# Kernel tuning notes

Hardware: AMD Instinct MI355X
Metric: run time of the kernel (lower is better)

## Reference

```python
import jax, jax.numpy as jnp
import numpy as np

# Production-scale dims (see shape_source)
B, L, K = 4096, 5, 32            # batch, hyperedge length (col0=cell id), neighbors/row
N = B * (L - 1)                  # aggregation rows = 16384
U, V = 131072, 500000            # unique neighbor nodes, embedding vocab (total bins)
F, E = 256, 256                  # feat_dim, embed_dim


def setup_inputs() -> dict:
    key = jax.random.key(0)
    ks = jax.random.split(key, 6)
    nodes = jax.random.randint(ks[0], (B, L), 0, V)                      # [B,L] int
    mask_row = jnp.repeat(jnp.arange(N, dtype=jnp.int32), K)             # [N*K] COO rows
    mask_col = jax.random.randint(ks[1], (N * K,), 0, U)                 # [N*K] COO cols
    mask_val = jnp.full((N * K,), 1.0 / K, dtype=jnp.float32)            # mean weights 1/deg
    unique_nodes = jax.random.randint(ks[2], (U,), 0, V)                 # [U] node ids
    embed_table = jax.random.normal(ks[3], (V, F), dtype=jnp.float32) * 0.02
    W = jax.random.normal(ks[4], (E, 2 * F), dtype=jnp.float32) / np.sqrt(2 * F)
    b = jnp.zeros((E,), dtype=jnp.float32)
    return dict(nodes=nodes, mask_row=mask_row, mask_col=mask_col, mask_val=mask_val,
                unique_nodes=unique_nodes, embed_table=embed_table, W=W, b=b)


def reference(nodes, mask_row, mask_col, mask_val, unique_nodes, embed_table, W, b):
    sz_b, len_seq = nodes.shape
    nodes_flat = nodes[:, 1:].reshape(-1)                                # [N]
    # MeanAggregator_with_weights: embed_matrix = features(unique_nodes)
    embed_matrix = embed_table[unique_nodes]                             # [U,F]
    # mask.mm(embed_matrix): COO spmm == gather + weighted segment-sum
    gathered = embed_matrix[mask_col] * mask_val[:, None]                # [nnz,F]
    neigh_feats = jax.ops.segment_sum(gathered, mask_row, num_segments=N)  # [N,F]
    # gcn=False -> concat self features (GraphSAGE-style)
    self_feats = embed_table[nodes_flat]                                 # [N,F]
    combined = jnp.concatenate([neigh_feats, self_feats], axis=-1)       # [N,2F]
    # swish(Linear(combined))
    h = combined @ W.T + b
    h = h * jax.nn.sigmoid(h)                                            # swish
    h = h.reshape(sz_b, len_seq - 1, -1)                                 # [B,L-1,E]
    # cell features from column 0, prepended
    cell_feats = embed_table[nodes[:, 0]]                                # [B,F]
    return jnp.concatenate([cell_feats[:, None, :], h], axis=1)          # [B,L,E]
```

## Files before the change

kernel.cpp:

```cpp
#include <hip/hip_runtime.h>
#include <math.h>

typedef float f4     __attribute__((ext_vector_type(4)));
typedef float f32x4  __attribute__((ext_vector_type(4)));
typedef short bf16x8 __attribute__((ext_vector_type(8)));
typedef unsigned short u16x4 __attribute__((ext_vector_type(4)));
typedef unsigned int   u32x4 __attribute__((ext_vector_type(4)));

#define NROWS   16384
#define KNEI    32
#define FDIM    256
#define TWOF    512
#define EDIM    256
#define BATCH   4096
#define UROWS   131072
#define BM      32

static __device__ __forceinline__ unsigned short f2bf(float x) {
    union { float f; unsigned int i; } c; c.f = x;
    unsigned int u = c.i;
    u += 0x7fffu + ((u >> 16) & 1u);
    return (unsigned short)(u >> 16);
}


#define EMBED_PB   2048
#define CELL_PB    64
#define WCONV_PB   8
#define ROWS_PW    16

__global__ __launch_bounds__(256) void prep_kernel(
    const int* __restrict__ unique_nodes, const float* __restrict__ table,
    const int* __restrict__ nodes, const float* __restrict__ W,
    unsigned short* __restrict__ embed4, float* __restrict__ scales,
    float* __restrict__ out, unsigned short* __restrict__ Wb)
{
    const int wave = threadIdx.x >> 6;
    const int lane = threadIdx.x & 63;
    const int blk  = blockIdx.x;

    if (blk < EMBED_PB) {
        const int u0 = (blk * 4 + wave) * ROWS_PW;
        #pragma unroll 2
        for (int t = 0; t < ROWS_PW; ++t) {
            const int u   = u0 + t;
            const int row = unique_nodes[u];
            const f4 e = *(const f4*)(table + (size_t)row * FDIM + lane * 4);
            float m = fmaxf(fmaxf(fabsf(e[0]), fabsf(e[1])),
                            fmaxf(fabsf(e[2]), fabsf(e[3])));
            #pragma unroll
            for (int s = 1; s < 64; s <<= 1)
                m = fmaxf(m, __shfl_xor(m, s));
            m = fmaxf(m, 1e-30f);
            const float inv = 7.0f / m;
            unsigned short pk = 0;
            #pragma unroll
            for (int j = 0; j < 4; ++j) {
                float qf = __builtin_rintf(e[j] * inv);
                qf = fminf(fmaxf(qf, -7.0f), 7.0f);
                const int q = (int)qf;
                pk |= (unsigned short)((q & 0xF) << (4 * j));
            }
            embed4[((size_t)u << 6) + lane] = pk;
            if (lane == 0) scales[u] = m * (1.0f / 7.0f);
        }
    } else if (blk < EMBED_PB + CELL_PB) {
        const int b0 = ((blk - EMBED_PB) * 4 + wave) * ROWS_PW;
        #pragma unroll 4
        for (int t = 0; t < ROWS_PW; ++t) {
            const int b = b0 + t;
            const int node = nodes[b * 5];
            const f4 e = *(const f4*)(table + (size_t)node * FDIM + lane * 4);
            *(f4*)(out + (size_t)b * 5 * FDIM + lane * 4) = e;
        }
    } else {
        const int base = (blk - EMBED_PB - CELL_PB) * 256 * 16 + threadIdx.x;
        #pragma unroll 4
        for (int t = 0; t < 16; ++t) {
            const int idx = base + t * 256;
            const f4 w = *(const f4*)(W + (size_t)idx * 4);
            u16x4 o;
            #pragma unroll
            for (int j = 0; j < 4; ++j) o[j] = f2bf(w[j]);
            *(u16x4*)(Wb + (size_t)idx * 4) = o;
        }
    }
}

__global__ __launch_bounds__(512, 4) void fused_kernel(
    const int* __restrict__ mask_col, const float* __restrict__ mask_val,
    const unsigned int* __restrict__ embed4, const float* __restrict__ scales,
    const int* __restrict__ nodes, const float* __restrict__ table,
    const unsigned short* __restrict__ Wb, const float* __restrict__ bias,
    float* __restrict__ out)
{
    __shared__ unsigned short As[BM * TWOF];
    char* const As_b = (char*)As;

    const int wave  = threadIdx.x >> 6;
    const int lane  = threadIdx.x & 63;
    const int half  = lane >> 5;
    const int l32   = lane & 31;
    const int rbase = blockIdx.x * BM;

    #pragma unroll
    for (int p = 0; p < 2; ++p) {
        const int lr = wave * 4 + p * 2;
        const int gi = rbase + lr;

        const int j   = gi * KNEI + lane;
        const int col = mask_col[j];
        const float val = mask_val[j] * scales[col];

        const int i_g = gi + half;
        const int nfr = nodes[(i_g >> 2) * 5 + 1 + (i_g & 3)];
        const float* sp = table + (size_t)nfr * FDIM + l32 * 8;
        const f4 s0 = *(const f4*)sp;
        const f4 s1 = *(const f4*)(sp + 4);

        f4 accA = (f4){0.f,0.f,0.f,0.f};
        f4 accB = (f4){0.f,0.f,0.f,0.f};
        #pragma unroll 8
        for (int k = 0; k < KNEI; ++k) {
            const int   c = __shfl(col, (lane & 32) + k);
            const float v = __shfl(val, (lane & 32) + k);
            const unsigned int w = embed4[((size_t)c << 5) + l32];
            #pragma unroll
            for (int d = 0; d < 4; ++d) {
                const int qa = ((int)(w << (28 - 4 * d))) >> 28;
                const int qb = ((int)(w << (12 - 4 * d))) >> 28;
                accA[d] += v * (float)qa;
                accB[d] += v * (float)qb;
            }
        }

        const int lrow = lr + half;
        const int swz  = (lrow & 7) << 4;

        u32x4 on;
        on[0] = (unsigned)f2bf(accA[0]) | ((unsigned)f2bf(accA[1]) << 16);
        on[1] = (unsigned)f2bf(accA[2]) | ((unsigned)f2bf(accA[3]) << 16);
        on[2] = (unsigned)f2bf(accB[0]) | ((unsigned)f2bf(accB[1]) << 16);
        on[3] = (unsigned)f2bf(accB[2]) | ((unsigned)f2bf(accB[3]) << 16);
        *(u32x4*)(As_b + lrow * 1024 + ((l32 * 16) ^ swz)) = on;

        u32x4 os;
        os[0] = (unsigned)f2bf(s0[0]) | ((unsigned)f2bf(s0[1]) << 16);
        os[1] = (unsigned)f2bf(s0[2]) | ((unsigned)f2bf(s0[3]) << 16);
        os[2] = (unsigned)f2bf(s1[0]) | ((unsigned)f2bf(s1[1]) << 16);
        os[3] = (unsigned)f2bf(s1[2]) | ((unsigned)f2bf(s1[3]) << 16);
        *(u32x4*)(As_b + lrow * 1024 + ((512 + l32 * 16) ^ swz)) = os;
    }

    __syncthreads();

    const int n_w    = wave * 32;
    const int lrow16 = lane & 15;
    const int koff   = (lane >> 4) * 8;
    const int aswz   = (lrow16 & 7) << 4;

    f32x4 acc[2][2] = {};
    const unsigned short* wp = Wb + (size_t)(n_w + lrow16) * TWOF + koff;

    #pragma unroll 4
    for (int kb = 0; kb < TWOF; kb += 32) {
        const int kbyte = (koff + kb) * 2;
        const bf16x8 a0 = *(const bf16x8*)(As_b + (lrow16     ) * 1024 + (kbyte ^ aswz));
        const bf16x8 a1 = *(const bf16x8*)(As_b + (lrow16 + 16) * 1024 + (kbyte ^ aswz));
        const bf16x8 b0 = *(const bf16x8*)(wp + kb);
        const bf16x8 b1 = *(const bf16x8*)(wp + 16 * TWOF + kb);
        acc[0][0] = __builtin_amdgcn_mfma_f32_16x16x32_bf16(a0, b0, acc[0][0], 0, 0, 0);
        acc[0][1] = __builtin_amdgcn_mfma_f32_16x16x32_bf16(a0, b1, acc[0][1], 0, 0, 0);
        acc[1][0] = __builtin_amdgcn_mfma_f32_16x16x32_bf16(a1, b0, acc[1][0], 0, 0, 0);
        acc[1][1] = __builtin_amdgcn_mfma_f32_16x16x32_bf16(a1, b1, acc[1][1], 0, 0, 0);
    }

    float bn[2];
    #pragma unroll
    for (int ni = 0; ni < 2; ++ni) bn[ni] = bias[n_w + ni * 16 + lrow16];

    #pragma unroll
    for (int mi = 0; mi < 2; ++mi) {
        #pragma unroll
        for (int ni = 0; ni < 2; ++ni) {
            const int n = n_w + ni * 16 + lrow16;
            #pragma unroll
            for (int j = 0; j < 4; ++j) {
                const int i = rbase + mi * 16 + (lane >> 4) * 4 + j;
                float h = acc[mi][ni][j] + bn[ni];
                h = h / (1.0f + __expf(-h));
                out[((size_t)(i >> 2) * 5 + 1 + (i & 3)) * FDIM + n] = h;
            }
        }
    }
}

__global__ __launch_bounds__(256) void neigh_f32_kernel(
    const int* __restrict__ mask_col, const float* __restrict__ mask_val,
    const int* __restrict__ unique_nodes, const float* __restrict__ table,
    float* __restrict__ neigh)
{
    const int wave = threadIdx.x >> 6;
    const int lane = threadIdx.x & 63;
    const int i = blockIdx.x * 4 + wave;
    int   row_l = 0;
    float val_l = 0.0f;
    if (lane < KNEI) {
        const int j = i * KNEI + lane;
        const int c = mask_col[j];
        val_l = mask_val[j];
        row_l = unique_nodes[c];
    }
    f4 acc = (f4){0.f, 0.f, 0.f, 0.f};
    #pragma unroll 8
    for (int k = 0; k < KNEI; ++k) {
        const int   row = __shfl(row_l, k);
        const float v   = __shfl(val_l, k);
        const f4 e = *(const f4*)(table + (size_t)row * FDIM + lane * 4);
        acc += v * e;
    }
    *(f4*)(neigh + (size_t)i * FDIM + lane * 4) = acc;
}

__global__ __launch_bounds__(256) void cell_kernel(
    const int* __restrict__ nodes, const float* __restrict__ table,
    float* __restrict__ out)
{
    const int wave = threadIdx.x >> 6;
    const int lane = threadIdx.x & 63;
    const int b = blockIdx.x * 4 + wave;
    const int node = nodes[b * 5];
    const f4 e = *(const f4*)(table + (size_t)node * FDIM + lane * 4);
    *(f4*)(out + (size_t)b * 5 * FDIM + lane * 4) = e;
}

__global__ __launch_bounds__(256) void gemm_f32_kernel(
    const float* __restrict__ neigh, const float* __restrict__ table,
    const int* __restrict__ nodes, const float* __restrict__ W,
    const float* __restrict__ bias, float* __restrict__ out)
{
    __shared__ float Asf[16][64];
    __shared__ float Wsf[16][64];
    const int t  = threadIdx.x;
    const int i0 = blockIdx.x * 64;
    const int e0 = blockIdx.y * 64;
    const int r  = t >> 2;
    const int k4 = (t & 3) << 2;
    const int irow = i0 + r;
    const int nfr = nodes[(irow >> 2) * 5 + 1 + (irow & 3)];
    const int tm = (t >> 4) << 2;
    const int tn = (t & 15) << 2;
    float acc[4][4] = {};
    for (int kb = 0; kb < TWOF; kb += 16) {
        const float* asrc = (kb < FDIM)
            ? (neigh + (size_t)irow * FDIM + kb + k4)
            : (table + (size_t)nfr  * FDIM + (kb - FDIM) + k4);
        const f4 av = *(const f4*)asrc;
        const f4 wv = *(const f4*)(W + (size_t)(e0 + r) * TWOF + kb + k4);
        __syncthreads();
        #pragma unroll
        for (int j = 0; j < 4; ++j) { Asf[k4 + j][r] = av[j]; Wsf[k4 + j][r] = wv[j]; }
        __syncthreads();
        #pragma unroll
        for (int k = 0; k < 16; ++k) {
            const f4 a = *(const f4*)&Asf[k][tm];
            const f4 w = *(const f4*)&Wsf[k][tn];
            #pragma unroll
            for (int mi = 0; mi < 4; ++mi)
                #pragma unroll
                for (int ni = 0; ni < 4; ++ni)
                    acc[mi][ni] += a[mi] * w[ni];
        }
    }
    #pragma unroll
    for (int mi = 0; mi < 4; ++mi) {
        const int i  = i0 + tm + mi;
        float* op = out + ((size_t)(i >> 2) * 5 + 1 + (i & 3)) * FDIM + e0 + tn;
        f4 hv;
        #pragma unroll
        for (int ni = 0; ni < 4; ++ni) {
            const float h = acc[mi][ni] + bias[e0 + tn + ni];
            hv[ni] = h / (1.0f + __expf(-h));
        }
        *(f4*)op = hv;
    }
}

extern "C" void kernel_launch(void* const* d_in, const int* in_sizes, int n_in,
                              void* d_out, int out_size, void* d_ws, size_t ws_size,
                              hipStream_t stream)
{
    const int*   nodes        = (const int*)  d_in[0];
    const int*   mask_col     = (const int*)  d_in[2];
    const float* mask_val     = (const float*)d_in[3];
    const int*   unique_nodes = (const int*)  d_in[4];
    const float* table        = (const float*)d_in[5];
    const float* W            = (const float*)d_in[6];
    const float* bias         = (const float*)d_in[7];
    float*       out          = (float*)d_out;

    const size_t EMBED4_B = (size_t)UROWS * 128;
    const size_t SC_B     = (size_t)UROWS * 4;
    const size_t W_B      = (size_t)EDIM  * TWOF * 2;

    if (ws_size >= EMBED4_B + SC_B + W_B) {
        unsigned short* embed4 = (unsigned short*)d_ws;
        float*          scales = (float*)((char*)d_ws + EMBED4_B);
        unsigned short* Wb     = (unsigned short*)((char*)d_ws + EMBED4_B + SC_B);

        prep_kernel<<<EMBED_PB + CELL_PB + WCONV_PB, 256, 0, stream>>>(
            unique_nodes, table, nodes, W, embed4, scales, out, Wb);
        fused_kernel<<<NROWS / BM, 512, 0, stream>>>(
            mask_col, mask_val, (const unsigned int*)embed4, scales,
            nodes, table, Wb, bias, out);
    } else {
        float* neigh = (float*)d_ws;
        neigh_f32_kernel<<<NROWS / 4, 256, 0, stream>>>(mask_col, mask_val,
                                                        unique_nodes, table, neigh);
        cell_kernel     <<<BATCH / 4, 256, 0, stream>>>(nodes, table, out);
        gemm_f32_kernel <<<dim3(NROWS / 64, EDIM / 64), 256, 0, stream>>>(
            neigh, table, nodes, W, bias, out);
    }
}
```

Measured before the change: 60.52 us.

## Fuse prep and main kernels with a grid barrier and offset-encoded int4 decode

Merges the embedding quantization, cell-feature copy and W-to-bf16 conversion into the main fused kernel. Each block does its share of prep work, then all blocks wait on a global atomic-counter barrier before the aggregation and GEMM phase. The int4 packing now stores nibbles with a +8 offset in an interleaved layout, so decoding is a mask-and-shift instead of sign-extending shifts; the offset is removed afterwards using the sum of the weights. The barrier assumes all 512 blocks are resident at once and adds a memset launch plus spin-wait cost.

```diff
diff --git a/kernel.cpp b/kernel.cpp
--- a/kernel.cpp
+++ b/kernel.cpp
@@ -15,6 +15,7 @@
 #define BATCH   4096
 #define UROWS   131072
 #define BM      32
+#define NBLK    (NROWS / BM)
 
 static __device__ __forceinline__ unsigned short f2bf(float x) {
     union { float f; unsigned int i; } c; c.f = x;
@@ -23,85 +24,79 @@
     return (unsigned short)(u >> 16);
 }
 
-
-#define EMBED_PB   2048
-#define CELL_PB    64
-#define WCONV_PB   8
-#define ROWS_PW    16
-
-__global__ __launch_bounds__(256) void prep_kernel(
-    const int* __restrict__ unique_nodes, const float* __restrict__ table,
-    const int* __restrict__ nodes, const float* __restrict__ W,
-    unsigned short* __restrict__ embed4, float* __restrict__ scales,
-    float* __restrict__ out, unsigned short* __restrict__ Wb)
-{
+__global__ __launch_bounds__(512, 4) void mega_kernel(
+    const int* __restrict__ mask_col, const float* __restrict__ mask_val,
+    const int* __restrict__ unique_nodes, const int* __restrict__ nodes,
+    const float* __restrict__ table, const float* __restrict__ W,
+    const float* __restrict__ bias,
+    unsigned int* __restrict__ embed4, float* __restrict__ scales,
+    unsigned short* __restrict__ Wb, unsigned int* __restrict__ ctrl,
+    float* __restrict__ out)
+{
+    __shared__ unsigned short As[BM * TWOF];
+    char* const As_b = (char*)As;
+
+    const int bid  = blockIdx.x;
     const int wave = threadIdx.x >> 6;
     const int lane = threadIdx.x & 63;
-    const int blk  = blockIdx.x;
-
-    if (blk < EMBED_PB) {
-        const int u0 = (blk * 4 + wave) * ROWS_PW;
+    const int half = lane >> 5;
+    const int l32  = lane & 31;
+
+    {
+        const int u0 = bid * 256 + wave * 32;
         #pragma unroll 2
-        for (int t = 0; t < ROWS_PW; ++t) {
-            const int u   = u0 + t;
+        for (int t = 0; t < 16; ++t) {
+            const int u   = u0 + t * 2 + half;
             const int row = unique_nodes[u];
-            const f4 e = *(const f4*)(table + (size_t)row * FDIM + lane * 4);
-            float m = fmaxf(fmaxf(fabsf(e[0]), fabsf(e[1])),
-                            fmaxf(fabsf(e[2]), fabsf(e[3])));
-            #pragma unroll
-            for (int s = 1; s < 64; s <<= 1)
-                m = fmaxf(m, __shfl_xor(m, s));
+            const float* rp = table + (size_t)row * FDIM + l32 * 8;
+            const f4 e0 = *(const f4*)rp;
+            const f4 e1 = *(const f4*)(rp + 4);
+            float m = fmaxf(
+                fmaxf(fmaxf(fabsf(e0[0]), fabsf(e0[1])), fmaxf(fabsf(e0[2]), fabsf(e0[3]))),
+                fmaxf(fmaxf(fabsf(e1[0]), fabsf(e1[1])), fmaxf(fabsf(e1[2]), fabsf(e1[3]))));
+            #pragma unroll
+            for (int s = 1; s < 32; s <<= 1) m = fmaxf(m, __shfl_xor(m, s));
             m = fmaxf(m, 1e-30f);
             const float inv = 7.0f / m;
-            unsigned short pk = 0;
+            unsigned int w = 0;
             #pragma unroll
             for (int j = 0; j < 4; ++j) {
-                float qf = __builtin_rintf(e[j] * inv);
-                qf = fminf(fmaxf(qf, -7.0f), 7.0f);
-                const int q = (int)qf;
-                pk |= (unsigned short)((q & 0xF) << (4 * j));
+                const int q0 = (int)fminf(fmaxf(__builtin_rintf(e0[j] * inv), -7.f), 7.f) + 8;
+                const int q1 = (int)fminf(fmaxf(__builtin_rintf(e1[j] * inv), -7.f), 7.f) + 8;
+                w |= (unsigned int)q0 << (8 * j);
+                w |= (unsigned int)q1 << (8 * j + 4);
             }
-            embed4[((size_t)u << 6) + lane] = pk;
-            if (lane == 0) scales[u] = m * (1.0f / 7.0f);
-        }
-    } else if (blk < EMBED_PB + CELL_PB) {
-        const int b0 = ((blk - EMBED_PB) * 4 + wave) * ROWS_PW;
-        #pragma unroll 4
-        for (int t = 0; t < ROWS_PW; ++t) {
-            const int b = b0 + t;
-            const int node = nodes[b * 5];
-            const f4 e = *(const f4*)(table + (size_t)node * FDIM + lane * 4);
-            *(f4*)(out + (size_t)b * 5 * FDIM + lane * 4) = e;
-        }
-    } else {
-        const int base = (blk - EMBED_PB - CELL_PB) * 256 * 16 + threadIdx.x;
-        #pragma unroll 4
-        for (int t = 0; t < 16; ++t) {
-            const int idx = base + t * 256;
-            const f4 w = *(const f4*)(W + (size_t)idx * 4);
+            embed4[((size_t)u << 5) + l32] = w;
+            if (l32 == 0) scales[u] = m * (1.0f / 7.0f);
+        }
+
+        const int b = bid * 8 + wave;
+        const int node = nodes[b * 5];
+        const f4 e = *(const f4*)(table + (size_t)node * FDIM + lane * 4);
+        *(f4*)(out + (size_t)b * 5 * FDIM + lane * 4) = e;
+
+        if (wave == 0) {
+            const int idx = bid * 64 + lane;
+            const f4 wv = *(const f4*)(W + (size_t)idx * 4);
             u16x4 o;
             #pragma unroll
-            for (int j = 0; j < 4; ++j) o[j] = f2bf(w[j]);
+            for (int j = 0; j < 4; ++j) o[j] = f2bf(wv[j]);
             *(u16x4*)(Wb + (size_t)idx * 4) = o;
         }
     }
-}
-
-__global__ __launch_bounds__(512, 4) void fused_kernel(
-    const int* __restrict__ mask_col, const float* __restrict__ mask_val,
-    const unsigned int* __restrict__ embed4, const float* __restrict__ scales,
-    const int* __restrict__ nodes, const float* __restrict__ table,
-    const unsigned short* __restrict__ Wb, const float* __restrict__ bias,
-    float* __restrict__ out)
-{
-    __shared__ unsigned short As[BM * TWOF];
-    char* const As_b = (char*)As;
-
-    const int wave  = threadIdx.x >> 6;
-    const int lane  = threadIdx.x & 63;
-    const int half  = lane >> 5;
-    const int l32   = lane & 31;
-    const int rbase = blockIdx.x * BM;
+
+    __syncthreads();
+    if (threadIdx.x == 0) {
+        __hip_atomic_fetch_add(&ctrl[0], 1u, __ATOMIC_RELEASE,
+                               __HIP_MEMORY_SCOPE_AGENT);
+        while (__hip_atomic_fetch_add(&ctrl[0], 0u, __ATOMIC_RELAXED,
+                                      __HIP_MEMORY_SCOPE_AGENT) < (unsigned)NBLK)
+            __builtin_amdgcn_s_sleep(16);
+        __builtin_amdgcn_fence(__ATOMIC_ACQUIRE, "agent");
+    }
+    __syncthreads();
+
+    const int rbase = bid * BM;
 
     #pragma unroll
     for (int p = 0; p < 2; ++p) {
@@ -120,19 +115,27 @@
 
         f4 accA = (f4){0.f,0.f,0.f,0.f};
         f4 accB = (f4){0.f,0.f,0.f,0.f};
+        float vsum = 0.0f;
         #pragma unroll 8
         for (int k = 0; k < KNEI; ++k) {
             const int   c = __shfl(col, (lane & 32) + k);
             const float v = __shfl(val, (lane & 32) + k);
-            const unsigned int w = embed4[((size_t)c << 5) + l32];
-            #pragma unroll
-            for (int d = 0; d < 4; ++d) {
-                const int qa = ((int)(w << (28 - 4 * d))) >> 28;
-                const int qb = ((int)(w << (12 - 4 * d))) >> 28;
-                accA[d] += v * (float)qa;
-                accB[d] += v * (float)qb;
-            }
-        }
+            const unsigned int w  = embed4[((size_t)c << 5) + l32];
+            const unsigned int lo =  w       & 0x0F0F0F0Fu;
+            const unsigned int hi = (w >> 4) & 0x0F0F0F0Fu;
+            accA[0] += v * (float)( lo        & 0xFFu);
+            accA[1] += v * (float)((lo >>  8) & 0xFFu);
+            accA[2] += v * (float)((lo >> 16) & 0xFFu);
+            accA[3] += v * (float)( lo >> 24        );
+            accB[0] += v * (float)( hi        & 0xFFu);
+            accB[1] += v * (float)((hi >>  8) & 0xFFu);
+            accB[2] += v * (float)((hi >> 16) & 0xFFu);
+            accB[3] += v * (float)( hi >> 24        );
+            vsum += v;
+        }
+        const float c8 = 8.0f * vsum;
+        #pragma unroll
+        for (int d = 0; d < 4; ++d) { accA[d] -= c8; accB[d] -= c8; }
 
         const int lrow = lr + half;
         const int swz  = (lrow & 7) << 4;
@@ -302,17 +305,18 @@
     const size_t EMBED4_B = (size_t)UROWS * 128;
     const size_t SC_B     = (size_t)UROWS * 4;
     const size_t W_B      = (size_t)EDIM  * TWOF * 2;
-
-    if (ws_size >= EMBED4_B + SC_B + W_B) {
-        unsigned short* embed4 = (unsigned short*)d_ws;
+    const size_t CTRL_B   = 128;
+
+    if (ws_size >= EMBED4_B + SC_B + W_B + CTRL_B) {
+        unsigned int*   embed4 = (unsigned int*)d_ws;
         float*          scales = (float*)((char*)d_ws + EMBED4_B);
         unsigned short* Wb     = (unsigned short*)((char*)d_ws + EMBED4_B + SC_B);
-
-        prep_kernel<<<EMBED_PB + CELL_PB + WCONV_PB, 256, 0, stream>>>(
-            unique_nodes, table, nodes, W, embed4, scales, out, Wb);
-        fused_kernel<<<NROWS / BM, 512, 0, stream>>>(
-            mask_col, mask_val, (const unsigned int*)embed4, scales,
-            nodes, table, Wb, bias, out);
+        unsigned int*   ctrl   = (unsigned int*)((char*)d_ws + EMBED4_B + SC_B + W_B);
+
+        (void)hipMemsetAsync(ctrl, 0, CTRL_B, stream);
+        mega_kernel<<<NBLK, 512, 0, stream>>>(
+            mask_col, mask_val, unique_nodes, nodes, table, W, bias,
+            embed4, scales, Wb, ctrl, out);
     } else {
         float* neigh = (float*)d_ws;
         neigh_f32_kernel<<<NROWS / 4, 256, 0, stream>>>(mask_col, mask_val,
```

Measured after the change: 108.3 us. 79.0% more time.
